# Optimization experiments

Hardware: AMD Instinct MI355X
Metric: run time of the kernel (lower is better)

The kernel has to match this reference:

```python
import jax, jax.numpy as jnp
import numpy as np

N = 100000      # nodes
E = 1600000     # edges (before self-loops)
IN_DIM = 32
HID = 64        # per-head channels of conv1
H1 = 2          # heads of conv1
OUT = 64        # conv2 out channels, heads=1
LN_EPS = 1e-5
NEG_SLOPE = 0.2   # PyG GATConv default LeakyReLU slope


def setup_inputs() -> dict:
    key = jax.random.key(0)
    ks = jax.random.split(key, 13)
    g = lambda k, shape, sc=0.1: (jax.random.normal(k, shape, jnp.float32) * sc)
    return {
        "x": jax.random.normal(ks[0], (N, IN_DIM), jnp.float32),
        "edge_index": jax.random.randint(ks[1], (2, E), 0, N, dtype=jnp.int32),
        # conv1: heads=2, out=HID -> lin weight [IN_DIM, H1*HID], att [H1, HID]
        "W1": g(ks[2], (IN_DIM, H1 * HID)),
        "att_src1": g(ks[3], (H1, HID)),
        "att_dst1": g(ks[4], (H1, HID)),
        "bias1": jnp.zeros((H1 * HID,), jnp.float32),
        # LayerNorm over 128 features
        "gamma": jnp.ones((H1 * HID,), jnp.float32),
        "beta": jnp.zeros((H1 * HID,), jnp.float32),
        # conv2: heads=1, in=128, out=OUT
        "W2": g(ks[5], (H1 * HID, OUT)),
        "att_src2": g(ks[6], (1, OUT)),
        "att_dst2": g(ks[7], (1, OUT)),
        "bias2": jnp.zeros((OUT,), jnp.float32),
    }


def gat_layer(x, src, dst, W, att_src, att_dst, bias, heads, out_ch, n):
    """PyG GATConv (shared src/dst lin, add_self_loops handled by caller)."""
    h = (x @ W).reshape(n, heads, out_ch)                 # [N,H,C]
    a_s = jnp.einsum('nhc,hc->nh', h, att_src)            # [N,H]
    a_d = jnp.einsum('nhc,hc->nh', h, att_dst)
    e = jax.nn.leaky_relu(a_s[src] + a_d[dst], NEG_SLOPE) # [E,H]
    # segment softmax over incoming edges of each destination node
    emax = jax.ops.segment_max(e, dst, num_segments=n)    # [N,H]
    e = jnp.exp(e - emax[dst])
    esum = jax.ops.segment_sum(e, dst, num_segments=n)
    alpha = e / (esum[dst] + 1e-16)                       # [E,H]
    msg = h[src] * alpha[:, :, None]                      # [E,H,C]
    out = jax.ops.segment_sum(msg, dst, num_segments=n)   # [N,H,C]
    return out.reshape(n, heads * out_ch) + bias


def reference(x, edge_index, W1, att_src1, att_dst1, bias1, gamma, beta,
              W2, att_src2, att_dst2, bias2):
    n = x.shape[0]
    loops = jnp.arange(n, dtype=edge_index.dtype)
    src = jnp.concatenate([edge_index[0], loops])         # add self-loops
    dst = jnp.concatenate([edge_index[1], loops])

    h = gat_layer(x, src, dst, W1, att_src1, att_dst1, bias1, H1, HID, n)
    # LayerNorm over feature dim, then ReLU
    mu = h.mean(-1, keepdims=True)
    var = ((h - mu) ** 2).mean(-1, keepdims=True)
    h = (h - mu) * jax.lax.rsqrt(var + LN_EPS) * gamma + beta
    h = jax.nn.relu(h)

    return gat_layer(h, src, dst, W2, att_src2, att_dst2, bias2, 1, OUT, n)
```

## Files before the change

kernel.cpp:

```cpp
#include <hip/hip_runtime.h>
#include <hip/hip_bf16.h>
#include <hip/hip_fp16.h>

#define IN_DIM 32
#define HID 64
#define H1 2
#define F1 (H1 * HID)
#define OUT_CH 64
#define NEG_SLOPE 0.2f
#define LN_EPS 1e-5f

#define BSHIFT 9
#define BMASK ((1 << BSHIFT) - 1)
#define CHUNK 4096
#define CAP 10240

typedef __attribute__((ext_vector_type(8))) short short8x;
typedef __attribute__((ext_vector_type(4))) float floatx4;
typedef __attribute__((ext_vector_type(2))) float floatx2;

__device__ __forceinline__ float leaky(float x) {
    return x > 0.f ? x : NEG_SLOPE * x;
}
__device__ __forceinline__ float bf2f(__hip_bfloat16 v) { return __bfloat162float(v); }
__device__ __forceinline__ short f2bs(float v) {
    __hip_bfloat16 t = __float2bfloat16(v);
    return *reinterpret_cast<short*>(&t);
}
__device__ __forceinline__ unsigned pack_bf16x2(float lo, float hi) {
    unsigned ul = (unsigned)(unsigned short)f2bs(lo);
    unsigned uh = (unsigned)(unsigned short)f2bs(hi);
    return (uh << 16) | ul;
}
__device__ __forceinline__ float bfu_lo(unsigned u) { return __uint_as_float(u << 16); }
__device__ __forceinline__ float bfu_hi(unsigned u) { return __uint_as_float(u & 0xffff0000u); }
__device__ __forceinline__ void pk_fma(floatx2& c, floatx2 a, floatx2 b) {
    asm("v_pk_fma_f32 %0, %1, %2, %0" : "+v"(c) : "v"(a), "v"(b));
}

__global__ __launch_bounds__(256) void k_bucket_pack(const int* __restrict__ src,
                                                     const int* __restrict__ dst,
                                                     int E, int nb, int nchunk,
                                                     int* __restrict__ bfill,
                                                     unsigned int* __restrict__ bedge,
                                                     const float* __restrict__ W1,
                                                     const float* __restrict__ W2,
                                                     const float* __restrict__ att_s,
                                                     const float* __restrict__ att_d,
                                                     __hip_bfloat16* __restrict__ W1t,
                                                     __hip_bfloat16* __restrict__ W2t,
                                                     float* __restrict__ wsd) {
    int t = threadIdx.x;
    if ((int)blockIdx.x >= nchunk) {
        int idx = ((int)blockIdx.x - nchunk) * 256 + t;
        if (idx < IN_DIM * F1) {
            int ch = idx >> 5, k = idx & 31;
            W1t[idx] = __float2bfloat16(W1[k * F1 + ch]);
        }
        if (idx < F1 * OUT_CH) {
            int ch = idx >> 7, k = idx & 127;
            W2t[idx] = __float2bfloat16(W2[k * OUT_CH + ch]);
        }
        if (idx < 128) {
            int v = idx >> 5;
            int k = idx & 31;
            const float* att = (v & 2) ? att_d : att_s;
            int h = v & 1;
            float s = 0.f;
#pragma unroll 8
            for (int c = 0; c < HID; c++)
                s = fmaf(W1[k * F1 + h * HID + c], att[h * HID + c], s);
            wsd[v * 32 + k] = s;
        }
        return;
    }
    __shared__ int h[512];
    __shared__ int gb[512];
    for (int i = t; i < nb; i += 256) h[i] = 0;
    __syncthreads();
    int base = blockIdx.x * CHUNK;
    unsigned int pk[16];
    int rk[16], bk[16];
#pragma unroll
    for (int j = 0; j < 16; j++) {
        int e = base + j * 256 + t;
        if (e < E) {
            int d = dst[e];
            int b = d >> BSHIFT;
            bk[j] = b;
            pk[j] = ((unsigned)src[e] << BSHIFT) | (unsigned)(d & BMASK);
            rk[j] = atomicAdd(&h[b], 1);
        } else bk[j] = -1;
    }
    __syncthreads();
    for (int i = t; i < nb; i += 256)
        gb[i] = h[i] ? atomicAdd(&bfill[i], h[i]) : 0;
    __syncthreads();
#pragma unroll
    for (int j = 0; j < 16; j++)
        if (bk[j] >= 0) {
            int pos = gb[bk[j]] + rk[j];
            if (pos < CAP) bedge[(size_t)bk[j] * CAP + pos] = pk[j];
        }
}

__global__ __launch_bounds__(256) void k_csr_att1(const unsigned int* __restrict__ bedge,
                                                  const int* __restrict__ bfill, int n, int nb,
                                                  int* __restrict__ cnt,
                                                  int* __restrict__ rowptr,
                                                  int* __restrict__ col,
                                                  const float* __restrict__ x,
                                                  const float* __restrict__ wsd,
                                                  __hip_bfloat16* __restrict__ xb16,
                                                  float2* __restrict__ as1,
                                                  float2* __restrict__ ad1) {
    int t = threadIdx.x;
    if ((int)blockIdx.x >= nb) {
        int node = ((int)blockIdx.x - nb) * 256 + t;
        if (node >= n) return;
        const float4* xp = (const float4*)(x + (size_t)node * IN_DIM);
        float4 xr[8];
#pragma unroll
        for (int i = 0; i < 8; i++) xr[i] = xp[i];
        const float* xf = (const float*)xr;
        short8x* xo = (short8x*)(xb16 + (size_t)node * IN_DIM);
#pragma unroll
        for (int i = 0; i < 4; i++) {
            short8x xb;
#pragma unroll
            for (int j = 0; j < 8; j++) xb[j] = f2bs(xf[i * 8 + j]);
            xo[i] = xb;
        }
        float d0 = 0.f, d1 = 0.f, d2 = 0.f, d3 = 0.f;
#pragma unroll
        for (int k = 0; k < 32; k++) {
            float xv = xf[k];
            d0 = fmaf(xv, wsd[k], d0);
            d1 = fmaf(xv, wsd[32 + k], d1);
            d2 = fmaf(xv, wsd[64 + k], d2);
            d3 = fmaf(xv, wsd[96 + k], d3);
        }
        as1[node] = make_float2(d0, d1);
        ad1[node] = make_float2(d2, d3);
        return;
    }
    int b = blockIdx.x;
    __shared__ int lcnt[512];
    __shared__ int lscan[256];
    int nbase = b << BSHIFT;
    lcnt[2 * t] = 0; lcnt[2 * t + 1] = 0;
    __syncthreads();
    int estart = b * CAP;
    int eend = estart + min(bfill[b], CAP);
    for (int e = estart + t; e < eend; e += 256)
        atomicAdd(&lcnt[bedge[e] & BMASK], 1);
    __syncthreads();
    int c0 = lcnt[2 * t], c1 = lcnt[2 * t + 1];
    int s = c0 + c1;
    lscan[t] = s;
    __syncthreads();
    for (int off = 1; off < 256; off <<= 1) {
        int u = (t >= off) ? lscan[t - off] : 0;
        __syncthreads();
        lscan[t] += u;
        __syncthreads();
    }
    int ex = lscan[t] - s;
    int node0 = nbase + 2 * t, node1 = node0 + 1;
    if (node0 < n) { cnt[node0] = c0; rowptr[node0] = estart + ex; }
    if (node1 < n) { cnt[node1] = c1; rowptr[node1] = estart + ex + c0; }
    __syncthreads();
    lcnt[2 * t] = ex;
    lcnt[2 * t + 1] = ex + c0;
    __syncthreads();
    for (int e = estart + t; e < eend; e += 256) {
        unsigned int p = bedge[e];
        int pos = estart + atomicAdd(&lcnt[p & BMASK], 1);
        col[pos] = (int)(p >> BSHIFT);
    }
}

__global__ __launch_bounds__(256) void k_agg1x(const __hip_bfloat16* __restrict__ xb16,
                                               const float2* __restrict__ as1p,
                                               const float2* __restrict__ ad1p,
                                               const int* __restrict__ rowptr,
                                               const int* __restrict__ cnt,
                                               const int* __restrict__ col,
                                               __hip_bfloat16* __restrict__ a, int n) {
    int wave = threadIdx.x >> 6;
    int lane = threadIdx.x & 63;
    int g = lane >> 3;
    int gl = lane & 7;
    int node = blockIdx.x * 32 + wave * 8 + g;
    bool valid = node < n;
    int nc = valid ? node : 0;
    float2 adn = ad1p[nc];
    float2 asn = as1p[nc];
    const unsigned* xu = (const unsigned*)xb16;
    float w0 = __expf(leaky(asn.x + adn.x));
    float w1 = __expf(leaky(asn.y + adn.y));
    uint2 su = *(const uint2*)(xu + (size_t)nc * 16 + gl * 2);
    float s0 = bfu_lo(su.x), s1 = bfu_hi(su.x), s2 = bfu_lo(su.y), s3 = bfu_hi(su.y);
    floatx2 acc0 = {w0 * s0, w1 * s0};
    floatx2 acc1 = {w0 * s1, w1 * s1};
    floatx2 acc2 = {w0 * s2, w1 * s2};
    floatx2 acc3 = {w0 * s3, w1 * s3};
    float ws0 = w0, ws1 = w1;
    int start = valid ? rowptr[nc] : 0;
    int deg = valid ? cnt[nc] : 0;
    int mx = deg;
    mx = max(mx, __shfl_xor(mx, 8, 64));
    mx = max(mx, __shfl_xor(mx, 16, 64));
    mx = max(mx, __shfl_xor(mx, 32, 64));
    int gbase = g << 3;
    for (int base = 0; base < mx; base += 8) {
        int m = deg - base;
        int colv = 0; unsigned wvv = 0u;
        float e0 = 0.f, e1 = 0.f;
        if (gl < m) {
            colv = col[start + base + gl];
            float2 as = as1p[colv];
            e0 = __expf(leaky(as.x + adn.x));
            e1 = __expf(leaky(as.y + adn.y));
            wvv = ((unsigned)__half_as_ushort(__float2half(e1)) << 16)
                | (unsigned)__half_as_ushort(__float2half(e0));
        }
        float r0 = e0, r1 = e1;
#pragma unroll
        for (int off = 1; off < 8; off <<= 1) {
            r0 += __shfl_xor(r0, off, 64);
            r1 += __shfl_xor(r1, off, 64);
        }
        ws0 += r0; ws1 += r1;
        int kend = min(8, mx - base);
        int k = 0;
        for (; k + 8 <= kend; k += 8) {
            int sx[8]; unsigned uw[8];
#pragma unroll
            for (int q = 0; q < 8; q++) {
                sx[q] = __shfl(colv, gbase + q);
                uw[q] = __shfl(wvv, gbase + q);
            }
            uint2 gu[8];
#pragma unroll
            for (int q = 0; q < 8; q++)
                gu[q] = *(const uint2*)(xu + (size_t)sx[q] * 16 + gl * 2);
#pragma unroll
            for (int q = 0; q < 8; q++) {
                float ww0 = __half2float(__ushort_as_half((unsigned short)(uw[q] & 0xffffu)));
                float ww1 = __half2float(__ushort_as_half((unsigned short)(uw[q] >> 16)));
                floatx2 wp = {ww0, ww1};
                floatx2 g0 = {bfu_lo(gu[q].x), bfu_lo(gu[q].x)};
                floatx2 g1 = {bfu_hi(gu[q].x), bfu_hi(gu[q].x)};
                floatx2 g2 = {bfu_lo(gu[q].y), bfu_lo(gu[q].y)};
                floatx2 g3 = {bfu_hi(gu[q].y), bfu_hi(gu[q].y)};
                pk_fma(acc0, wp, g0);
                pk_fma(acc1, wp, g1);
                pk_fma(acc2, wp, g2);
                pk_fma(acc3, wp, g3);
            }
        }
        for (; k < kend; k++) {
            int s = __shfl(colv, gbase + k);
            unsigned u = __shfl(wvv, gbase + k);
            uint2 u2 = *(const uint2*)(xu + (size_t)s * 16 + gl * 2);
            float ww0 = __half2float(__ushort_as_half((unsigned short)(u & 0xffffu)));
            float ww1 = __half2float(__ushort_as_half((unsigned short)(u >> 16)));
            floatx2 wp = {ww0, ww1};
            floatx2 g0 = {bfu_lo(u2.x), bfu_lo(u2.x)};
            floatx2 g1 = {bfu_hi(u2.x), bfu_hi(u2.x)};
            floatx2 g2 = {bfu_lo(u2.y), bfu_lo(u2.y)};
            floatx2 g3 = {bfu_hi(u2.y), bfu_hi(u2.y)};
            pk_fma(acc0, wp, g0);
            pk_fma(acc1, wp, g1);
            pk_fma(acc2, wp, g2);
            pk_fma(acc3, wp, g3);
        }
    }
    if (valid) {
        float inv0 = 1.f / (ws0 + 1e-16f);
        float inv1 = 1.f / (ws1 + 1e-16f);
        uint2 o0, o1;
        o0.x = pack_bf16x2(acc0.x * inv0, acc1.x * inv0);
        o0.y = pack_bf16x2(acc2.x * inv0, acc3.x * inv0);
        o1.x = pack_bf16x2(acc0.y * inv1, acc1.y * inv1);
        o1.y = pack_bf16x2(acc2.y * inv1, acc3.y * inv1);
        *(uint2*)(a + (size_t)node * 64 + 4 * gl) = o0;
        *(uint2*)(a + (size_t)node * 64 + 32 + 4 * gl) = o1;
    }
}

__global__ __launch_bounds__(256) void k_ln1node2(const __hip_bfloat16* __restrict__ a,
                                                  const __hip_bfloat16* __restrict__ W1t,
                                                  const float* __restrict__ bias1,
                                                  const float* __restrict__ gamma,
                                                  const float* __restrict__ beta,
                                                  const __hip_bfloat16* __restrict__ W2t,
                                                  const float* __restrict__ att_s2,
                                                  const float* __restrict__ att_d2,
                                                  __hip_bfloat16* __restrict__ h2b,
                                                  float* __restrict__ as2,
                                                  float* __restrict__ ad2, int n) {
    __shared__ __hip_bfloat16 hs[64][136];
    int wave = threadIdx.x >> 6;
    int lane = threadIdx.x & 63;
    int row16 = lane & 15;
    int quad = lane >> 4;
    int node0 = blockIdx.x * 64 + wave * 16;

    {
        short8x bfr[8];
#pragma unroll
        for (int nt = 0; nt < 8; nt++)
            bfr[nt] = *(const short8x*)(W1t + (nt * 16 + row16) * IN_DIM + quad * 8);

        int arow = node0 + row16;
        if (arow >= n) arow = n - 1;
        const __hip_bfloat16* ap = a + (size_t)arow * 64 + quad * 8;
        short8x af0 = *(const short8x*)ap;
        short8x af1 = *(const short8x*)(ap + 32);

        floatx4 acc[8];
#pragma unroll
        for (int nt = 0; nt < 8; nt++) acc[nt] = (floatx4){0.f, 0.f, 0.f, 0.f};
#pragma unroll
        for (int nt = 0; nt < 8; nt++)
            acc[nt] = __builtin_amdgcn_mfma_f32_16x16x32_bf16(nt < 4 ? af0 : af1, bfr[nt],
                                                              acc[nt], 0, 0, 0);

        float bv[8], gv[8], btv[8];
#pragma unroll
        for (int nt = 0; nt < 8; nt++) {
            int ch = nt * 16 + row16;
            bv[nt] = bias1[ch];
            gv[nt] = gamma[ch];
            btv[nt] = beta[ch];
        }
#pragma unroll
        for (int rr = 0; rr < 4; rr++) {
            int node = node0 + quad * 4 + rr;
            float v[8];
            float sum = 0.f, sq = 0.f;
#pragma unroll
            for (int nt = 0; nt < 8; nt++) {
                v[nt] = acc[nt][rr] + bv[nt];
                sum += v[nt];
                sq += v[nt] * v[nt];
            }
#pragma unroll
            for (int off = 1; off < 16; off <<= 1) {
                sum += __shfl_xor(sum, off, 64);
                sq += __shfl_xor(sq, off, 64);
            }
            float mu = sum * (1.f / 128.f);
            float var = sq * (1.f / 128.f) - mu * mu;
            float r = rsqrtf(var + LN_EPS);
            if (node < n) {
                int lr = wave * 16 + quad * 4 + rr;
#pragma unroll
                for (int nt = 0; nt < 8; nt++) {
                    float o = (v[nt] - mu) * r * gv[nt] + btv[nt];
                    hs[lr][nt * 16 + row16] = __float2bfloat16(fmaxf(o, 0.f));
                }
            }
        }
    }
    __syncthreads();

    short8x bfr2[4][4];
#pragma unroll
    for (int nt = 0; nt < 4; nt++) {
        const __hip_bfloat16* wrow = W2t + (nt * 16 + row16) * F1 + quad * 8;
#pragma unroll
        for (int kc = 0; kc < 4; kc++)
            bfr2[kc][nt] = *(const short8x*)(wrow + kc * 32);
    }

    floatx4 acc2[4];
#pragma unroll
    for (int nt = 0; nt < 4; nt++) acc2[nt] = (floatx4){0.f, 0.f, 0.f, 0.f};

    int lrow = wave * 16 + row16;
#pragma unroll
    for (int kc = 0; kc < 4; kc++) {
        short8x af = *(const short8x*)&hs[lrow][quad * 8 + kc * 32];
#pragma unroll
        for (int nt = 0; nt < 4; nt++)
            acc2[nt] = __builtin_amdgcn_mfma_f32_16x16x32_bf16(af, bfr2[kc][nt], acc2[nt],
                                                               0, 0, 0);
    }

    float asv[4], adv[4];
#pragma unroll
    for (int nt = 0; nt < 4; nt++) {
        asv[nt] = att_s2[nt * 16 + row16];
        adv[nt] = att_d2[nt * 16 + row16];
    }
#pragma unroll
    for (int rr = 0; rr < 4; rr++) {
        int node = node0 + quad * 4 + rr;
        float ps = 0.f, pd = 0.f;
#pragma unroll
        for (int nt = 0; nt < 4; nt++) {
            float v = acc2[nt][rr];
            if (node < n) h2b[(size_t)node * OUT_CH + nt * 16 + row16] = __float2bfloat16(v);
            ps = fmaf(v, asv[nt], ps);
            pd = fmaf(v, adv[nt], pd);
        }
#pragma unroll
        for (int off = 1; off < 16; off <<= 1) {
            ps += __shfl_xor(ps, off, 64);
            pd += __shfl_xor(pd, off, 64);
        }
        if (row16 == 0 && node < n) { as2[node] = ps; ad2[node] = pd; }
    }
}

__global__ __launch_bounds__(256) void k_agg2(const __hip_bfloat16* __restrict__ h2b,
                                              const float* __restrict__ as2,
                                              const float* __restrict__ ad2,
                                              const int* __restrict__ rowptr,
                                              const int* __restrict__ cnt,
                                              const int* __restrict__ col,
                                              const float* __restrict__ bias2,
                                              float* __restrict__ out, int n) {
    int wave = threadIdx.x >> 6;
    int lane = threadIdx.x & 63;
    int g = lane >> 3;
    int gl = lane & 7;
    int node = blockIdx.x * 32 + wave * 8 + g;
    bool valid = node < n;
    int nc = valid ? node : 0;
    const unsigned* h2u = (const unsigned*)h2b;
    float adn = ad2[nc];
    float wself = __expf(leaky(as2[nc] + adn));
    uint4 su = *(const uint4*)(h2u + (size_t)nc * 32 + gl * 4);
    floatx2 acc0 = {wself * bfu_lo(su.x), wself * bfu_hi(su.x)};
    floatx2 acc1 = {wself * bfu_lo(su.y), wself * bfu_hi(su.y)};
    floatx2 acc2 = {wself * bfu_lo(su.z), wself * bfu_hi(su.z)};
    floatx2 acc3 = {wself * bfu_lo(su.w), wself * bfu_hi(su.w)};
    float wsum = wself;
    int start = valid ? rowptr[nc] : 0;
    int deg = valid ? cnt[nc] : 0;
    int mx = deg;
    mx = max(mx, __shfl_xor(mx, 8, 64));
    mx = max(mx, __shfl_xor(mx, 16, 64));
    mx = max(mx, __shfl_xor(mx, 32, 64));
    int gbase = g << 3;
    for (int base = 0; base < mx; base += 8) {
        int m = deg - base;
        int colv = 0; float wvv = 0.f;
        if (gl < m) {
            colv = col[start + base + gl];
            wvv = __expf(leaky(as2[colv] + adn));
        }
        float r = wvv;
#pragma unroll
        for (int off = 1; off < 8; off <<= 1) r += __shfl_xor(r, off, 64);
        wsum += r;
        int kend = min(8, mx - base);
        int k = 0;
        for (; k + 4 <= kend; k += 4) {
            int sx[4]; float wx[4];
#pragma unroll
            for (int q = 0; q < 4; q++) {
                sx[q] = __shfl(colv, gbase + k + q);
                wx[q] = __shfl(wvv, gbase + k + q);
            }
            uint4 gu[4];
#pragma unroll
            for (int q = 0; q < 4; q++)
                gu[q] = *(const uint4*)(h2u + (size_t)sx[q] * 32 + gl * 4);
#pragma unroll
            for (int q = 0; q < 4; q++) {
                floatx2 wp = {wx[q], wx[q]};
                floatx2 g0 = {bfu_lo(gu[q].x), bfu_hi(gu[q].x)};
                floatx2 g1 = {bfu_lo(gu[q].y), bfu_hi(gu[q].y)};
                floatx2 g2 = {bfu_lo(gu[q].z), bfu_hi(gu[q].z)};
                floatx2 g3 = {bfu_lo(gu[q].w), bfu_hi(gu[q].w)};
                pk_fma(acc0, wp, g0);
                pk_fma(acc1, wp, g1);
                pk_fma(acc2, wp, g2);
                pk_fma(acc3, wp, g3);
            }
        }
        for (; k < kend; k++) {
            int s = __shfl(colv, gbase + k);
            float wk = __shfl(wvv, gbase + k);
            uint4 u4 = *(const uint4*)(h2u + (size_t)s * 32 + gl * 4);
            floatx2 wp = {wk, wk};
            floatx2 g0 = {bfu_lo(u4.x), bfu_hi(u4.x)};
            floatx2 g1 = {bfu_lo(u4.y), bfu_hi(u4.y)};
            floatx2 g2 = {bfu_lo(u4.z), bfu_hi(u4.z)};
            floatx2 g3 = {bfu_lo(u4.w), bfu_hi(u4.w)};
            pk_fma(acc0, wp, g0);
            pk_fma(acc1, wp, g1);
            pk_fma(acc2, wp, g2);
            pk_fma(acc3, wp, g3);
        }
    }
    if (valid) {
        float inv = 1.f / (wsum + 1e-16f);
        const float4* bp = (const float4*)bias2;
        float4 bv0 = bp[gl * 2], bv1 = bp[gl * 2 + 1];
        float4 ov0, ov1;
        ov0.x = acc0.x * inv + bv0.x;
        ov0.y = acc0.y * inv + bv0.y;
        ov0.z = acc1.x * inv + bv0.z;
        ov0.w = acc1.y * inv + bv0.w;
        ov1.x = acc2.x * inv + bv1.x;
        ov1.y = acc2.y * inv + bv1.y;
        ov1.z = acc3.x * inv + bv1.z;
        ov1.w = acc3.y * inv + bv1.w;
        float4* op = (float4*)out + (size_t)node * 16 + gl * 2;
        op[0] = ov0;
        op[1] = ov1;
    }
}

extern "C" void kernel_launch(void* const* d_in, const int* in_sizes, int n_in,
                              void* d_out, int out_size, void* d_ws, size_t ws_size,
                              hipStream_t stream) {
    const float* x        = (const float*)d_in[0];
    const int*   eidx     = (const int*)d_in[1];
    const float* W1       = (const float*)d_in[2];
    const float* att_src1 = (const float*)d_in[3];
    const float* att_dst1 = (const float*)d_in[4];
    const float* bias1    = (const float*)d_in[5];
    const float* gamma    = (const float*)d_in[6];
    const float* beta     = (const float*)d_in[7];
    const float* W2       = (const float*)d_in[8];
    const float* att_src2 = (const float*)d_in[9];
    const float* att_dst2 = (const float*)d_in[10];
    const float* bias2    = (const float*)d_in[11];
    float* out = (float*)d_out;

    const int N = in_sizes[0] / IN_DIM;
    const int E = in_sizes[1] / 2;
    const int* src = eidx;
    const int* dst = eidx + E;
    const int nb = (N + BMASK) >> BSHIFT;

    char* w = (char*)d_ws;
    __hip_bfloat16* xb16  = (__hip_bfloat16*)w;  w += (size_t)N * IN_DIM * 2;
    __hip_bfloat16* a     = (__hip_bfloat16*)w;  w += (size_t)N * 64 * 2;
    __hip_bfloat16* h2b   = (__hip_bfloat16*)w;  w += (size_t)N * OUT_CH * 2;
    __hip_bfloat16* W1t   = (__hip_bfloat16*)w;  w += IN_DIM * F1 * 2;
    __hip_bfloat16* W2t   = (__hip_bfloat16*)w;  w += F1 * OUT_CH * 2;
    float* wsd = (float*)w; w += 128 * 4;
    float* as1 = (float*)w; w += (size_t)N * 2 * 4;
    float* ad1 = (float*)w; w += (size_t)N * 2 * 4;
    float* as2 = (float*)w; w += (size_t)N * 4;
    float* ad2 = (float*)w; w += (size_t)N * 4;
    int* cnt    = (int*)w; w += (size_t)N * 4;
    int* rowptr = (int*)w; w += (size_t)N * 4;
    int* bfill  = (int*)w; w += 512 * 4;
    int* col    = (int*)w; w += (size_t)nb * CAP * 4;
    unsigned int* bedge = (unsigned int*)w; w += (size_t)nb * CAP * 4;

    const int nchunk = (E + CHUNK - 1) / CHUNK;

    hipMemsetAsync(bfill, 0, 512 * 4, stream);
    k_bucket_pack<<<nchunk + 32, 256, 0, stream>>>(src, dst, E, nb, nchunk, bfill, bedge,
                                                   W1, W2, att_src1, att_dst1,
                                                   W1t, W2t, wsd);
    k_csr_att1<<<nb + (N + 255) / 256, 256, 0, stream>>>(bedge, bfill, N, nb,
                                                         cnt, rowptr, col,
                                                         x, wsd, xb16,
                                                         (float2*)as1, (float2*)ad1);
    k_agg1x<<<(N + 31) / 32, 256, 0, stream>>>(xb16, (const float2*)as1, (const float2*)ad1,
                                               rowptr, cnt, col, a, N);
    k_ln1node2<<<(N + 63) / 64, 256, 0, stream>>>(a, W1t, bias1, gamma, beta,
                                                  W2t, att_src2, att_dst2,
                                                  h2b, as2, ad2, N);
    k_agg2<<<(N + 31) / 32, 256, 0, stream>>>(h2b, as2, ad2,
                                              rowptr, cnt, col, bias2, out, N);
}
```

Baseline: 226.1 us.

## Fuse layer-1 aggregation with LayerNorm and layer-2 projection via shared memory

Merges the layer-1 edge aggregation kernel into the LayerNorm/linear kernel. Each 512-thread block aggregates 128 nodes into an LDS tile that is reused as the staging buffer for the MFMA stages. This removes the global round trip of the intermediate aggregated features and one kernel launch. The cost is larger blocks, a bigger LDS footprint and extra barriers, which may reduce occupancy for the gather-heavy aggregation phase.

```diff
diff --git a/kernel.cpp b/kernel.cpp
--- a/kernel.cpp
+++ b/kernel.cpp
@@ -180,145 +180,154 @@
     }
 }
 
-__global__ __launch_bounds__(256) void k_agg1x(const __hip_bfloat16* __restrict__ xb16,
-                                               const float2* __restrict__ as1p,
-                                               const float2* __restrict__ ad1p,
-                                               const int* __restrict__ rowptr,
-                                               const int* __restrict__ cnt,
-                                               const int* __restrict__ col,
-                                               __hip_bfloat16* __restrict__ a, int n) {
+__global__ __launch_bounds__(512) void k_agg1_ln(const __hip_bfloat16* __restrict__ xb16,
+                                                 const float2* __restrict__ as1p,
+                                                 const float2* __restrict__ ad1p,
+                                                 const int* __restrict__ rowptr,
+                                                 const int* __restrict__ cnt,
+                                                 const int* __restrict__ col,
+                                                 const __hip_bfloat16* __restrict__ W1t,
+                                                 const float* __restrict__ bias1,
+                                                 const float* __restrict__ gamma,
+                                                 const float* __restrict__ beta,
+                                                 const __hip_bfloat16* __restrict__ W2t,
+                                                 const float* __restrict__ att_s2,
+                                                 const float* __restrict__ att_d2,
+                                                 __hip_bfloat16* __restrict__ h2b,
+                                                 float* __restrict__ as2,
+                                                 float* __restrict__ ad2, int n) {
+    __shared__ char smem[128 * 136 * 2];
+    __hip_bfloat16 (*a_s)[68] = (__hip_bfloat16(*)[68])smem;
+    __hip_bfloat16 (*hs)[136] = (__hip_bfloat16(*)[136])smem;
+
     int wave = threadIdx.x >> 6;
     int lane = threadIdx.x & 63;
-    int g = lane >> 3;
-    int gl = lane & 7;
-    int node = blockIdx.x * 32 + wave * 8 + g;
-    bool valid = node < n;
-    int nc = valid ? node : 0;
-    float2 adn = ad1p[nc];
-    float2 asn = as1p[nc];
-    const unsigned* xu = (const unsigned*)xb16;
-    float w0 = __expf(leaky(asn.x + adn.x));
-    float w1 = __expf(leaky(asn.y + adn.y));
-    uint2 su = *(const uint2*)(xu + (size_t)nc * 16 + gl * 2);
-    float s0 = bfu_lo(su.x), s1 = bfu_hi(su.x), s2 = bfu_lo(su.y), s3 = bfu_hi(su.y);
-    floatx2 acc0 = {w0 * s0, w1 * s0};
-    floatx2 acc1 = {w0 * s1, w1 * s1};
-    floatx2 acc2 = {w0 * s2, w1 * s2};
-    floatx2 acc3 = {w0 * s3, w1 * s3};
-    float ws0 = w0, ws1 = w1;
-    int start = valid ? rowptr[nc] : 0;
-    int deg = valid ? cnt[nc] : 0;
-    int mx = deg;
-    mx = max(mx, __shfl_xor(mx, 8, 64));
-    mx = max(mx, __shfl_xor(mx, 16, 64));
-    mx = max(mx, __shfl_xor(mx, 32, 64));
-    int gbase = g << 3;
-    for (int base = 0; base < mx; base += 8) {
-        int m = deg - base;
-        int colv = 0; unsigned wvv = 0u;
-        float e0 = 0.f, e1 = 0.f;
-        if (gl < m) {
-            colv = col[start + base + gl];
-            float2 as = as1p[colv];
-            e0 = __expf(leaky(as.x + adn.x));
-            e1 = __expf(leaky(as.y + adn.y));
-            wvv = ((unsigned)__half_as_ushort(__float2half(e1)) << 16)
-                | (unsigned)__half_as_ushort(__float2half(e0));
-        }
-        float r0 = e0, r1 = e1;
-#pragma unroll
-        for (int off = 1; off < 8; off <<= 1) {
-            r0 += __shfl_xor(r0, off, 64);
-            r1 += __shfl_xor(r1, off, 64);
-        }
-        ws0 += r0; ws1 += r1;
-        int kend = min(8, mx - base);
-        int k = 0;
-        for (; k + 8 <= kend; k += 8) {
-            int sx[8]; unsigned uw[8];
-#pragma unroll
-            for (int q = 0; q < 8; q++) {
-                sx[q] = __shfl(colv, gbase + q);
-                uw[q] = __shfl(wvv, gbase + q);
-            }
-            uint2 gu[8];
-#pragma unroll
-            for (int q = 0; q < 8; q++)
-                gu[q] = *(const uint2*)(xu + (size_t)sx[q] * 16 + gl * 2);
-#pragma unroll
-            for (int q = 0; q < 8; q++) {
-                float ww0 = __half2float(__ushort_as_half((unsigned short)(uw[q] & 0xffffu)));
-                float ww1 = __half2float(__ushort_as_half((unsigned short)(uw[q] >> 16)));
-                floatx2 wp = {ww0, ww1};
-                floatx2 g0 = {bfu_lo(gu[q].x), bfu_lo(gu[q].x)};
-                floatx2 g1 = {bfu_hi(gu[q].x), bfu_hi(gu[q].x)};
-                floatx2 g2 = {bfu_lo(gu[q].y), bfu_lo(gu[q].y)};
-                floatx2 g3 = {bfu_hi(gu[q].y), bfu_hi(gu[q].y)};
-                pk_fma(acc0, wp, g0);
-                pk_fma(acc1, wp, g1);
-                pk_fma(acc2, wp, g2);
-                pk_fma(acc3, wp, g3);
-            }
-        }
-        for (; k < kend; k++) {
-            int s = __shfl(colv, gbase + k);
-            unsigned u = __shfl(wvv, gbase + k);
-            uint2 u2 = *(const uint2*)(xu + (size_t)s * 16 + gl * 2);
-            float ww0 = __half2float(__ushort_as_half((unsigned short)(u & 0xffffu)));
-            float ww1 = __half2float(__ushort_as_half((unsigned short)(u >> 16)));
-            floatx2 wp = {ww0, ww1};
-            floatx2 g0 = {bfu_lo(u2.x), bfu_lo(u2.x)};
-            floatx2 g1 = {bfu_hi(u2.x), bfu_hi(u2.x)};
-            floatx2 g2 = {bfu_lo(u2.y), bfu_lo(u2.y)};
-            floatx2 g3 = {bfu_hi(u2.y), bfu_hi(u2.y)};
-            pk_fma(acc0, wp, g0);
-            pk_fma(acc1, wp, g1);
-            pk_fma(acc2, wp, g2);
-            pk_fma(acc3, wp, g3);
-        }
-    }
-    if (valid) {
-        float inv0 = 1.f / (ws0 + 1e-16f);
-        float inv1 = 1.f / (ws1 + 1e-16f);
-        uint2 o0, o1;
-        o0.x = pack_bf16x2(acc0.x * inv0, acc1.x * inv0);
-        o0.y = pack_bf16x2(acc2.x * inv0, acc3.x * inv0);
-        o1.x = pack_bf16x2(acc0.y * inv1, acc1.y * inv1);
-        o1.y = pack_bf16x2(acc2.y * inv1, acc3.y * inv1);
-        *(uint2*)(a + (size_t)node * 64 + 4 * gl) = o0;
-        *(uint2*)(a + (size_t)node * 64 + 32 + 4 * gl) = o1;
-    }
-}
-
-__global__ __launch_bounds__(256) void k_ln1node2(const __hip_bfloat16* __restrict__ a,
-                                                  const __hip_bfloat16* __restrict__ W1t,
-                                                  const float* __restrict__ bias1,
-                                                  const float* __restrict__ gamma,
-                                                  const float* __restrict__ beta,
-                                                  const __hip_bfloat16* __restrict__ W2t,
-                                                  const float* __restrict__ att_s2,
-                                                  const float* __restrict__ att_d2,
-                                                  __hip_bfloat16* __restrict__ h2b,
-                                                  float* __restrict__ as2,
-                                                  float* __restrict__ ad2, int n) {
-    __shared__ __hip_bfloat16 hs[64][136];
-    int wave = threadIdx.x >> 6;
-    int lane = threadIdx.x & 63;
+
+    {
+        int g = lane >> 3;
+        int gl = lane & 7;
+        const unsigned* xu = (const unsigned*)xb16;
+#pragma unroll
+        for (int half = 0; half < 2; half++) {
+            int lr = half * 64 + wave * 8 + g;
+            int node = blockIdx.x * 128 + lr;
+            bool valid = node < n;
+            int nc = valid ? node : 0;
+            float2 adn = ad1p[nc];
+            float2 asn = as1p[nc];
+            float w0 = __expf(leaky(asn.x + adn.x));
+            float w1 = __expf(leaky(asn.y + adn.y));
+            uint2 su = *(const uint2*)(xu + (size_t)nc * 16 + gl * 2);
+            float s0 = bfu_lo(su.x), s1 = bfu_hi(su.x), s2 = bfu_lo(su.y), s3 = bfu_hi(su.y);
+            floatx2 acc0 = {w0 * s0, w1 * s0};
+            floatx2 acc1 = {w0 * s1, w1 * s1};
+            floatx2 acc2 = {w0 * s2, w1 * s2};
+            floatx2 acc3 = {w0 * s3, w1 * s3};
+            float ws0 = w0, ws1 = w1;
+            int start = valid ? rowptr[nc] : 0;
+            int deg = valid ? cnt[nc] : 0;
+            int mx = deg;
+            mx = max(mx, __shfl_xor(mx, 8, 64));
+            mx = max(mx, __shfl_xor(mx, 16, 64));
+            mx = max(mx, __shfl_xor(mx, 32, 64));
+            int gbase = g << 3;
+            for (int base = 0; base < mx; base += 8) {
+                int m = deg - base;
+                int colv = 0; unsigned wvv = 0u;
+                float e0 = 0.f, e1 = 0.f;
+                if (gl < m) {
+                    colv = col[start + base + gl];
+                    float2 as = as1p[colv];
+                    e0 = __expf(leaky(as.x + adn.x));
+                    e1 = __expf(leaky(as.y + adn.y));
+                    wvv = ((unsigned)__half_as_ushort(__float2half(e1)) << 16)
+                        | (unsigned)__half_as_ushort(__float2half(e0));
+                }
+                float r0 = e0, r1 = e1;
+#pragma unroll
+                for (int off = 1; off < 8; off <<= 1) {
+                    r0 += __shfl_xor(r0, off, 64);
+                    r1 += __shfl_xor(r1, off, 64);
+                }
+                ws0 += r0; ws1 += r1;
+                int kend = min(8, mx - base);
+                int k = 0;
+                for (; k + 8 <= kend; k += 8) {
+                    int sx[8]; unsigned uw[8];
+#pragma unroll
+                    for (int q = 0; q < 8; q++) {
+                        sx[q] = __shfl(colv, gbase + q);
+                        uw[q] = __shfl(wvv, gbase + q);
+                    }
+                    uint2 gu[8];
+#pragma unroll
+                    for (int q = 0; q < 8; q++)
+                        gu[q] = *(const uint2*)(xu + (size_t)sx[q] * 16 + gl * 2);
+#pragma unroll
+                    for (int q = 0; q < 8; q++) {
+                        float ww0 = __half2float(__ushort_as_half((unsigned short)(uw[q] & 0xffffu)));
+                        float ww1 = __half2float(__ushort_as_half((unsigned short)(uw[q] >> 16)));
+                        floatx2 wp = {ww0, ww1};
+                        floatx2 g0 = {bfu_lo(gu[q].x), bfu_lo(gu[q].x)};
+                        floatx2 g1 = {bfu_hi(gu[q].x), bfu_hi(gu[q].x)};
+                        floatx2 g2 = {bfu_lo(gu[q].y), bfu_lo(gu[q].y)};
+                        floatx2 g3 = {bfu_hi(gu[q].y), bfu_hi(gu[q].y)};
+                        pk_fma(acc0, wp, g0);
+                        pk_fma(acc1, wp, g1);
+                        pk_fma(acc2, wp, g2);
+                        pk_fma(acc3, wp, g3);
+                    }
+                }
+                for (; k < kend; k++) {
+                    int s = __shfl(colv, gbase + k);
+                    unsigned u = __shfl(wvv, gbase + k);
+                    uint2 u2 = *(const uint2*)(xu + (size_t)s * 16 + gl * 2);
+                    float ww0 = __half2float(__ushort_as_half((unsigned short)(u & 0xffffu)));
+                    float ww1 = __half2float(__ushort_as_half((unsigned short)(u >> 16)));
+                    floatx2 wp = {ww0, ww1};
+                    floatx2 g0 = {bfu_lo(u2.x), bfu_lo(u2.x)};
+                    floatx2 g1 = {bfu_hi(u2.x), bfu_hi(u2.x)};
+                    floatx2 g2 = {bfu_lo(u2.y), bfu_lo(u2.y)};
+                    floatx2 g3 = {bfu_hi(u2.y), bfu_hi(u2.y)};
+                    pk_fma(acc0, wp, g0);
+                    pk_fma(acc1, wp, g1);
+                    pk_fma(acc2, wp, g2);
+                    pk_fma(acc3, wp, g3);
+                }
+            }
+            uint2 o0 = {0u, 0u}, o1 = {0u, 0u};
+            if (valid) {
+                float inv0 = 1.f / (ws0 + 1e-16f);
+                float inv1 = 1.f / (ws1 + 1e-16f);
+                o0.x = pack_bf16x2(acc0.x * inv0, acc1.x * inv0);
+                o0.y = pack_bf16x2(acc2.x * inv0, acc3.x * inv0);
+                o1.x = pack_bf16x2(acc0.y * inv1, acc1.y * inv1);
+                o1.y = pack_bf16x2(acc2.y * inv1, acc3.y * inv1);
+            }
+            *(uint2*)&a_s[lr][4 * gl] = o0;
+            *(uint2*)&a_s[lr][32 + 4 * gl] = o1;
+        }
+    }
+    __syncthreads();
+
     int row16 = lane & 15;
     int quad = lane >> 4;
-    int node0 = blockIdx.x * 64 + wave * 16;
+    int node0 = blockIdx.x * 128 + wave * 16;
+    int lrow = wave * 16 + row16;
+
+    short8x af0, af1;
+    {
+        const __hip_bfloat16* ap = &a_s[lrow][quad * 8];
+        af0 = *(const short8x*)ap;
+        af1 = *(const short8x*)(&a_s[lrow][32 + quad * 8]);
+    }
+    __syncthreads();
 
     {
         short8x bfr[8];
 #pragma unroll
         for (int nt = 0; nt < 8; nt++)
             bfr[nt] = *(const short8x*)(W1t + (nt * 16 + row16) * IN_DIM + quad * 8);
-
-        int arow = node0 + row16;
-        if (arow >= n) arow = n - 1;
-        const __hip_bfloat16* ap = a + (size_t)arow * 64 + quad * 8;
-        short8x af0 = *(const short8x*)ap;
-        short8x af1 = *(const short8x*)(ap + 32);
 
         floatx4 acc[8];
 #pragma unroll
@@ -355,13 +364,11 @@
             float mu = sum * (1.f / 128.f);
             float var = sq * (1.f / 128.f) - mu * mu;
             float r = rsqrtf(var + LN_EPS);
-            if (node < n) {
-                int lr = wave * 16 + quad * 4 + rr;
-#pragma unroll
-                for (int nt = 0; nt < 8; nt++) {
-                    float o = (v[nt] - mu) * r * gv[nt] + btv[nt];
-                    hs[lr][nt * 16 + row16] = __float2bfloat16(fmaxf(o, 0.f));
-                }
+            int lr2 = wave * 16 + quad * 4 + rr;
+#pragma unroll
+            for (int nt = 0; nt < 8; nt++) {
+                float o = (node < n) ? (v[nt] - mu) * r * gv[nt] + btv[nt] : 0.f;
+                hs[lr2][nt * 16 + row16] = __float2bfloat16(fmaxf(o, 0.f));
             }
         }
     }
@@ -380,7 +387,6 @@
 #pragma unroll
     for (int nt = 0; nt < 4; nt++) acc2[nt] = (floatx4){0.f, 0.f, 0.f, 0.f};
 
-    int lrow = wave * 16 + row16;
 #pragma unroll
     for (int kc = 0; kc < 4; kc++) {
         short8x af = *(const short8x*)&hs[lrow][quad * 8 + kc * 32];
@@ -543,7 +549,6 @@
 
     char* w = (char*)d_ws;
     __hip_bfloat16* xb16  = (__hip_bfloat16*)w;  w += (size_t)N * IN_DIM * 2;
-    __hip_bfloat16* a     = (__hip_bfloat16*)w;  w += (size_t)N * 64 * 2;
     __hip_bfloat16* h2b   = (__hip_bfloat16*)w;  w += (size_t)N * OUT_CH * 2;
     __hip_bfloat16* W1t   = (__hip_bfloat16*)w;  w += IN_DIM * F1 * 2;
     __hip_bfloat16* W2t   = (__hip_bfloat16*)w;  w += F1 * OUT_CH * 2;
@@ -568,11 +573,12 @@
                                                          cnt, rowptr, col,
                                                          x, wsd, xb16,
                                                          (float2*)as1, (float2*)ad1);
-    k_agg1x<<<(N + 31) / 32, 256, 0, stream>>>(xb16, (const float2*)as1, (const float2*)ad1,
-                                               rowptr, cnt, col, a, N);
-    k_ln1node2<<<(N + 63) / 64, 256, 0, stream>>>(a, W1t, bias1, gamma, beta,
-                                                  W2t, att_src2, att_dst2,
-                                                  h2b, as2, ad2, N);
+    k_agg1_ln<<<(N + 127) / 128, 512, 0, stream>>>(xb16, (const float2*)as1,
+                                                   (const float2*)ad1,
+                                                   rowptr, cnt, col,
+                                                   W1t, bias1, gamma, beta,
+                                                   W2t, att_src2, att_dst2,
+                                                   h2b, as2, ad2, N);
     k_agg2<<<(N + 31) / 32, 256, 0, stream>>>(h2b, as2, ad2,
                                               rowptr, cnt, col, bias2, out, N);
 }
```

Result: slower. 234.7 us (+3.8%).
